# Kernel optimization log

Measured on AMD Instinct MI355X. Metric: run time of the kernel, lower is better.

The kernel has to match this reference:

```python
import jax, jax.numpy as jnp
import numpy as np

N, E, G = 50000, 800000, 256
NODE_IN, EDGE_IN, H, L, RO, OUT = 64, 16, 128, 3, 128, 2
EPS = 1e-5


def _ln(x, g, b):
    m = jnp.mean(x, axis=-1, keepdims=True)
    v = jnp.mean((x - m) ** 2, axis=-1, keepdims=True)
    return (x - m) * jax.lax.rsqrt(v + EPS) * g + b


def setup_inputs() -> dict:
    key = jax.random.key(0)
    ks = iter(jax.random.split(key, 40))
    w = lambda *s: jax.random.normal(next(ks), s, dtype=jnp.float32) * 0.05
    inp = {
        "x": jax.random.normal(next(ks), (N, NODE_IN), dtype=jnp.float32),
        "edge_attr": jax.random.normal(next(ks), (E, EDGE_IN), dtype=jnp.float32),
        "edge_index": jax.random.randint(next(ks), (2, E), 0, N, dtype=jnp.int32),
        "batch": jnp.sort(jax.random.randint(next(ks), (N,), 0, G, dtype=jnp.int32)),
        # encoders + input norms
        "node_enc_w": w(NODE_IN, H), "node_enc_b": jnp.zeros((H,), jnp.float32),
        "edge_enc_w": w(EDGE_IN, H), "edge_enc_b": jnp.zeros((H,), jnp.float32),
        "node_ln_g": jnp.ones((H,), jnp.float32), "node_ln_b": jnp.zeros((H,), jnp.float32),
        "edge_ln_g": jnp.ones((H,), jnp.float32), "edge_ln_b": jnp.zeros((H,), jnp.float32),
        # per-layer stacked params [L, ...]
        "msg_w1": w(L, 2 * H, H), "msg_b1": jnp.zeros((L, H), jnp.float32),
        "msg_w2": w(L, H, H), "msg_b2": jnp.zeros((L, H), jnp.float32),
        "gate_w": w(L, 2 * H, H), "gate_b": jnp.zeros((L, H), jnp.float32),
        "res_w1": w(L, 2 * H, H), "res_b1": jnp.zeros((L, H), jnp.float32),
        "res_w2": w(L, H, H), "res_b2": jnp.zeros((L, H), jnp.float32),
        "ln_g": jnp.ones((L, H), jnp.float32), "ln_b": jnp.zeros((L, H), jnp.float32),
        # readout MLP
        "ro_w1": w(H, RO), "ro_b1": jnp.zeros((RO,), jnp.float32),
        "ro_w2": w(RO, OUT), "ro_b2": jnp.zeros((OUT,), jnp.float32),
    }
    return inp


def reference(x, edge_attr, edge_index, batch,
              node_enc_w, node_enc_b, edge_enc_w, edge_enc_b,
              node_ln_g, node_ln_b, edge_ln_g, edge_ln_b,
              msg_w1, msg_b1, msg_w2, msg_b2, gate_w, gate_b,
              res_w1, res_b1, res_w2, res_b2, ln_g, ln_b,
              ro_w1, ro_b1, ro_w2, ro_b2):
    src, dst = edge_index[0], edge_index[1]
    h = _ln(x @ node_enc_w + node_enc_b, node_ln_g, node_ln_b)        # [N,H]
    e = _ln(edge_attr @ edge_enc_w + edge_enc_b, edge_ln_g, edge_ln_b)  # [E,H]
    for l in range(L):
        cat = jnp.concatenate([h[src], e], axis=-1)                   # [E,2H]
        gate = jax.nn.sigmoid(cat @ gate_w[l] + gate_b[l])
        msg = jax.nn.relu(cat @ msg_w1[l] + msg_b1[l]) @ msg_w2[l] + msg_b2[l]
        agg = jax.ops.segment_sum(gate * msg, dst, num_segments=N)    # scatter-add
        comb = jnp.concatenate([h, agg], axis=-1)                     # [N,2H]
        res = jax.nn.relu(comb @ res_w1[l] + res_b1[l]) @ res_w2[l] + res_b2[l]
        h = _ln(h + res, ln_g[l], ln_b[l])
    # global mean pool over graphs
    sums = jax.ops.segment_sum(h, batch, num_segments=G)              # [G,H]
    cnt = jax.ops.segment_sum(jnp.ones((h.shape[0],), h.dtype), batch, num_segments=G)
    g = sums / jnp.maximum(cnt, 1.0)[:, None]
    return jax.nn.relu(g @ ro_w1 + ro_b1) @ ro_w2 + ro_b2             # [G,OUT]
```

## Files before the change

kernel.cpp:

```cpp
#include <hip/hip_runtime.h>
#include <hip/hip_bf16.h>
#include <math.h>

#define NN 50000
#define NE 800000
#define NG 256
#define H 128
#define NIN 64
#define EIN 16
#define NL 3
#define LEPS 1e-5f

typedef short bf16x8 __attribute__((ext_vector_type(8)));
typedef float f32x4 __attribute__((ext_vector_type(4)));
typedef float f32x16 __attribute__((ext_vector_type(16)));
typedef unsigned u32x4 __attribute__((ext_vector_type(4)));

__device__ __forceinline__ short bf16rne(float x) {
  unsigned u = __float_as_uint(x);
  unsigned r = u + 0x7fff + ((u >> 16) & 1);
  return (short)(r >> 16);
}

__device__ __forceinline__ unsigned pk2(float lo, float hi) {
  __hip_bfloat162 h = __float22bfloat162_rn(make_float2(lo, hi));
  return *(unsigned*)&h;
}

__device__ __forceinline__ float wsum(float v) {
#pragma unroll
  for (int m = 1; m < 64; m <<= 1) v += __shfl_xor(v, m, 64);
  return v;
}

__global__ __launch_bounds__(256) void k_count(const int* __restrict__ eidx,
                                               unsigned* __restrict__ cnt) {
  int t = blockIdx.x * 256 + threadIdx.x;
  if (t < NE) atomicAdd(&cnt[eidx[NE + t]], 1u);
}

__global__ __launch_bounds__(1024) void k_scan(const unsigned* __restrict__ cnt,
                                               unsigned* __restrict__ rowptr) {
  __shared__ unsigned part[16];
  __shared__ unsigned carry_s;
  const int tid = threadIdx.x, lane = tid & 63, wid = tid >> 6;
  if (tid == 0) carry_s = 0;
  __syncthreads();
  for (int base = 0; base < NN; base += 1024) {
    int i = base + tid;
    unsigned v = (i < NN) ? cnt[i] : 0u;
    unsigned incl = v;
#pragma unroll
    for (int off = 1; off < 64; off <<= 1) {
      unsigned t = __shfl_up(incl, off, 64);
      if (lane >= off) incl += t;
    }
    if (lane == 63) part[wid] = incl;
    __syncthreads();
    if (tid == 0) {
      unsigned s = 0;
#pragma unroll
      for (int w = 0; w < 16; w++) { unsigned t = part[w]; part[w] = s; s += t; }
    }
    __syncthreads();
    unsigned carry = carry_s;
    if (i < NN) rowptr[i] = carry + part[wid] + incl - v;
    __syncthreads();
    if (tid == 1023) carry_s = carry + part[15] + incl;
    __syncthreads();
  }
}

__global__ __launch_bounds__(256) void k_fold(
    const float* __restrict__ gate_w, const float* __restrict__ msg_w1,
    const float* __restrict__ gate_b, const float* __restrict__ msg_b1,
    const float* __restrict__ e_enc_w, const float* __restrict__ e_enc_b,
    const float* __restrict__ e_ln_g, const float* __restrict__ e_ln_b,
    short* __restrict__ w2e, float* __restrict__ stats) {
  const int S_W2E = 3 * 8192;
  const int S_ST = S_W2E + 290;
  int tid = blockIdx.x * 256 + threadIdx.x;
  if (tid >= S_ST) return;
  if (tid < S_W2E) {
    int l = tid / 8192, e = tid % 8192;
    int f = e >> 9, lane = (e >> 3) & 63, j = e & 7;
    int nt = f >> 1, ks2 = f & 1;
    int k = ks2 * 16 + (lane >> 5) * 8 + j;
    int n = nt * 32 + (lane & 31);
    float s = 0.f;
    if (k < 19) {
      for (int m = 0; m < 128; m++) {
        float w = (n < 128) ? gate_w[((size_t)l * 256 + 128 + m) * 128 + n]
                            : msg_w1[((size_t)l * 256 + 128 + m) * 128 + (n - 128)];
        float fm = (k < 16)   ? e_enc_w[k * 128 + m] * e_ln_g[m]
                 : (k == 16)  ? e_enc_b[m] * e_ln_g[m]
                 : (k == 17)  ? e_ln_g[m]
                              : e_ln_b[m];
        s += fm * w;
      }
      if (k == 18)
        s += (n < 128) ? gate_b[l * 128 + n] : msg_b1[l * 128 + (n - 128)];
    }
    w2e[tid] = bf16rne(s);
  } else {
    int e = tid - S_W2E;
    if (e < 256) {
      int i = e >> 4, j = e & 15;
      float s = 0.f;
      for (int n = 0; n < 128; n++)
        s += e_enc_w[i * 128 + n] * e_enc_w[j * 128 + n];
      stats[e] = s;
    } else if (e < 272) {
      int k = e - 256;
      float s = 0.f;
      for (int n = 0; n < 128; n++) s += e_enc_w[k * 128 + n];
      stats[e] = s;
    } else if (e < 288) {
      int k = e - 272;
      float s = 0.f;
      for (int n = 0; n < 128; n++) s += e_enc_w[k * 128 + n] * e_enc_b[n];
      stats[e] = s;
    } else if (e == 288) {
      float s = 0.f;
      for (int n = 0; n < 128; n++) s += e_enc_b[n] * e_enc_b[n];
      stats[e] = s;
    } else {
      float s = 0.f;
      for (int n = 0; n < 128; n++) s += e_enc_b[n];
      stats[e] = s;
    }
  }
}

__global__ __launch_bounds__(256) void k_scatter(
    const int* __restrict__ eidx, const float* __restrict__ ea,
    const unsigned* __restrict__ rowptr, unsigned* __restrict__ cursor,
    const float* __restrict__ stats,
    int* __restrict__ src_s, int* __restrict__ dst_s,
    short* __restrict__ ea_bf, float2* __restrict__ rsmu) {
  __shared__ float S[290];
  for (int i = threadIdx.x; i < 290; i += 256) S[i] = stats[i];
  __syncthreads();
  int t = blockIdx.x * 256 + threadIdx.x;
  int s = eidx[t], d = eidx[NE + t];
  unsigned pos = rowptr[d] + atomicAdd(&cursor[d], 1u);
  src_s[pos] = s;
  dst_s[pos] = d;
  const float4* er = (const float4*)(ea + (size_t)t * EIN);
  float4 q0 = er[0], q1 = er[1], q2 = er[2], q3 = er[3];
  float e16[16];
  e16[0]=q0.x; e16[1]=q0.y; e16[2]=q0.z; e16[3]=q0.w;
  e16[4]=q1.x; e16[5]=q1.y; e16[6]=q1.z; e16[7]=q1.w;
  e16[8]=q2.x; e16[9]=q2.y; e16[10]=q2.z; e16[11]=q2.w;
  e16[12]=q3.x; e16[13]=q3.y; e16[14]=q3.z; e16[15]=q3.w;
  short tmp[16];
#pragma unroll
  for (int j = 0; j < 16; j++) tmp[j] = bf16rne(e16[j]);
  short* dstp = ea_bf + (size_t)pos * EIN;
  *(bf16x8*)dstp = *(bf16x8*)tmp;
  *(bf16x8*)(dstp + 8) = *(bf16x8*)(tmp + 8);
  float s1 = S[289], s2 = S[288];
#pragma unroll
  for (int k = 0; k < 16; k++) {
    s1 = fmaf(e16[k], S[256 + k], s1);
    s2 = fmaf(2.f * e16[k], S[272 + k], s2);
  }
#pragma unroll
  for (int i = 0; i < 16; i++) {
    float mi = 0.f;
#pragma unroll
    for (int j = 0; j < 16; j++) mi = fmaf(S[i * 16 + j], e16[j], mi);
    s2 = fmaf(e16[i], mi, s2);
  }
  float mu = s1 * (1.f / 128.f);
  float var = s2 * (1.f / 128.f) - mu * mu;
  float rs = rsqrtf(var + LEPS);
  rsmu[pos] = make_float2(rs, mu);
}

__global__ __launch_bounds__(256) void k_convert_w(
    const float* __restrict__ gate_w, const float* __restrict__ msg_w1,
    const float* __restrict__ msg_w2, const float* __restrict__ res_w1,
    const float* __restrict__ res_w2,
    short* __restrict__ bgh, short* __restrict__ bm2,
    short* __restrict__ brs1, short* __restrict__ brs2) {
  const int S_BGH = 3 * 65536;
  const int S_BM2 = S_BGH + 3 * 16384;
  const int S_BR1 = S_BM2 + 3 * 32768;
  const int S_BR2 = S_BR1 + 3 * 16384;
  int tid = blockIdx.x * 256 + threadIdx.x;
  if (tid >= S_BR2) return;
  if (tid < S_BGH) {
    int l = tid / 65536, e = tid % 65536;
    int f = e >> 9, lane = (e >> 3) & 63, j = e & 7;
    int nt = f >> 4, ks = f & 15;
    int k = ks * 16 + (lane >> 5) * 8 + j;
    int n = nt * 32 + (lane & 31);
    float v = (n < 128) ? gate_w[((size_t)l * 256 + k) * 128 + n]
                        : msg_w1[((size_t)l * 256 + k) * 128 + (n - 128)];
    bgh[tid] = bf16rne(v);
  } else if (tid < S_BM2) {
    int e0 = tid - S_BGH;
    int l = e0 / 16384, e = e0 % 16384;
    int f = e >> 9, lane = (e >> 3) & 63, j = e & 7;
    int nt = f >> 3, ks = f & 7;
    int k = ks * 16 + (lane >> 5) * 8 + j;
    int n = nt * 32 + (lane & 31);
    bm2[e0] = bf16rne(msg_w2[((size_t)l * 128 + k) * 128 + n]);
  } else if (tid < S_BR1) {
    int e0 = tid - S_BM2;
    int l = e0 / 32768, e = e0 % 32768;
    int f = e >> 9, lane = (e >> 3) & 63, j = e & 7;
    int nt = f >> 3, ks = f & 7;
    int k = ks * 32 + (lane >> 4) * 8 + j;
    int n = nt * 16 + (lane & 15);
    brs1[e0] = bf16rne(res_w1[((size_t)l * 256 + k) * 128 + n]);
  } else {
    int e0 = tid - S_BR1;
    int l = e0 / 16384, e = e0 % 16384;
    int f = e >> 9, lane = (e >> 3) & 63, j = e & 7;
    int nt = f >> 2, ks = f & 3;
    int k = ks * 32 + (lane >> 4) * 8 + j;
    int n = nt * 16 + (lane & 15);
    brs2[e0] = bf16rne(res_w2[((size_t)l * 128 + k) * 128 + n]);
  }
}

__global__ __launch_bounds__(256) void k_node_encode(
    const float* __restrict__ x, const float* __restrict__ W,
    const float* __restrict__ bias,
    const float* __restrict__ lng, const float* __restrict__ lnb,
    float* __restrict__ h, short* __restrict__ h_bf) {
  __shared__ float xs[4][8 * NIN];
  const int wave = threadIdx.x >> 6, lane = threadIdx.x & 63;
  const int n0 = (blockIdx.x * 4 + wave) * 8;
  float* xt = xs[wave];
  for (int i = lane; i < 8 * NIN; i += 64) {
    int idx = n0 * NIN + i;
    xt[i] = (idx < NN * NIN) ? x[idx] : 0.f;
  }
  __syncthreads();
  const int c0 = lane, c1 = lane + 64;
  float a0[8], a1[8];
#pragma unroll
  for (int j = 0; j < 8; j++) { a0[j] = 0.f; a1[j] = 0.f; }
  for (int k = 0; k < NIN; k++) {
    float w0 = W[k * H + c0], w1 = W[k * H + c1];
#pragma unroll
    for (int j = 0; j < 8; j++) {
      float xv = xt[j * NIN + k];
      a0[j] = fmaf(xv, w0, a0[j]);
      a1[j] = fmaf(xv, w1, a1[j]);
    }
  }
  const float b0 = bias[c0], b1 = bias[c1];
  const float g0 = lng[c0], g1 = lng[c1], lb0 = lnb[c0], lb1 = lnb[c1];
#pragma unroll
  for (int j = 0; j < 8; j++) {
    float v0 = a0[j] + b0, v1 = a1[j] + b1;
    float mean = wsum(v0 + v1) * (1.f / H);
    float d0 = v0 - mean, d1 = v1 - mean;
    float var = wsum(d0 * d0 + d1 * d1) * (1.f / H);
    float rs = rsqrtf(var + LEPS);
    int n = n0 + j;
    if (n < NN) {
      float o0 = d0 * rs * g0 + lb0, o1 = d1 * rs * g1 + lb1;
      h[n * H + c0] = o0;
      h[n * H + c1] = o1;
      h_bf[n * H + c0] = bf16rne(o0);
      h_bf[n * H + c1] = bf16rne(o1);
    }
  }
}

__global__ __launch_bounds__(256) void k_edge_mfma(
    const short* __restrict__ ea_bf, const float2* __restrict__ rsmu,
    const int* __restrict__ src_s, const int* __restrict__ dst_s,
    const short* __restrict__ h_bf,
    const short* __restrict__ Bgh, const short* __restrict__ Bm2,
    const short* __restrict__ W2e, const float* __restrict__ mbias2,
    float* __restrict__ agg) {
  __shared__ short wbuf[2][4096];
  __shared__ short regn[4][32 * 136];
  __shared__ int dsts[4][32];
  const int tid = threadIdx.x;
  const int wave = tid >> 6, lane = tid & 63;
  const int xcd = blockIdx.x & 7, bidx = blockIdx.x >> 3;
  const int blk = (xcd < 2 ? xcd * 782 : 2 * 782 + (xcd - 2) * 781) + bidx;
  const int e0 = blk * 128 + wave * 32;
  short* R = regn[wave];
  float* Rf = (float*)R;
  const int c31 = lane & 31, halfl = lane >> 5;
  const int koff = halfl * 8;
  const int soff0 = (2 * wave) * 512 + lane * 8;
  const int soff1 = (2 * wave + 1) * 512 + lane * 8;

  if (lane < 32) dsts[wave][lane] = dst_s[e0 + lane];

  bf16x8 w2ef[16];
#pragma unroll
  for (int f = 0; f < 16; f++)
    w2ef[f] = *(const bf16x8*)(W2e + (size_t)(f * 64 + lane) * 8);
  float mb2v[4];
#pragma unroll
  for (int gt = 0; gt < 4; gt++) mb2v[gt] = mbias2[gt * 32 + c31];

  const int srow = src_s[e0 + c31];
  bf16x8 af[8];
#pragma unroll
  for (int ks = 0; ks < 8; ks++)
    af[ks] = *(const bf16x8*)(h_bf + (size_t)srow * H + ks * 16 + koff);

  const float2 rm = rsmu[e0 + c31];
  bf16x8 ae;
  {
    bf16x8 raw = *(const bf16x8*)(ea_bf + (size_t)(e0 + c31) * EIN + koff);
    u32x4 v;
#pragma unroll
    for (int p = 0; p < 4; p++) {
      float lo = __uint_as_float(((unsigned)(unsigned short)raw[2 * p]) << 16) * rm.x;
      float hi = __uint_as_float(((unsigned)(unsigned short)raw[2 * p + 1]) << 16) * rm.x;
      v[p] = pk2(lo, hi);
    }
    ae = __builtin_bit_cast(bf16x8, v);
  }
  bf16x8 ae2;
  {
    u32x4 w;
    w[0] = halfl ? 0u : pk2(rm.x, -rm.x * rm.y);
    w[1] = halfl ? 0u : 0x00003F80u;
    w[2] = 0u; w[3] = 0u;
    ae2 = __builtin_bit_cast(bf16x8, w);
  }

  {
    const short* s = Bgh + (size_t)4 * 8192;
    bf16x8 p0 = *(const bf16x8*)(s + soff0);
    bf16x8 p1 = *(const bf16x8*)(s + soff1);
    *(bf16x8*)&wbuf[0][soff0] = p0;
    *(bf16x8*)&wbuf[0][soff1] = p1;
  }
  __syncthreads();

  bf16x8 a2[8];
  float gate[16];
  bf16x8 sl0, sl1;

#pragma unroll
  for (int t = 0; t < 12; t++) {
    const int b = t & 1;
    if (t < 11) {
      const int tn = t + 1;
      const short* s;
      if (tn < 4) s = Bgh + (size_t)(4 + tn) * 8192;
      else if (((tn - 4) & 1) == 0) s = Bgh + (size_t)((tn - 4) >> 1) * 8192;
      else s = Bm2 + (size_t)((tn - 4) >> 1) * 4096;
      sl0 = *(const bf16x8*)(s + soff0);
      sl1 = *(const bf16x8*)(s + soff1);
    }
    if (t < 4) {
      const int nt = 4 + t;
      __builtin_amdgcn_s_setprio(1);
      f32x16 a = __builtin_amdgcn_mfma_f32_32x32x16_bf16(
          ae, w2ef[nt * 2], (f32x16)(0.f), 0, 0, 0);
      a = __builtin_amdgcn_mfma_f32_32x32x16_bf16(ae2, w2ef[nt * 2 + 1], a, 0, 0, 0);
#pragma unroll
      for (int ks = 0; ks < 8; ks++)
        a = __builtin_amdgcn_mfma_f32_32x32x16_bf16(
            af[ks], *(const bf16x8*)&wbuf[b][ks * 512 + lane * 8], a, 0, 0, 0);
      __builtin_amdgcn_s_setprio(0);
      const int col = t * 32 + c31;
#pragma unroll
      for (int r = 0; r < 16; r++) {
        int row = (r & 3) + 8 * (r >> 2) + 4 * halfl;
        R[row * 136 + col] = bf16rne(fmaxf(a[r], 0.f));
      }
      if (t == 3) {
#pragma unroll
        for (int ks = 0; ks < 8; ks++)
          a2[ks] = *(const bf16x8*)&R[c31 * 136 + ks * 16 + koff];
      }
    } else if (((t - 4) & 1) == 0) {
      const int gt = (t - 4) >> 1;
      __builtin_amdgcn_s_setprio(1);
      f32x16 a = __builtin_amdgcn_mfma_f32_32x32x16_bf16(
          ae, w2ef[gt * 2], (f32x16)(0.f), 0, 0, 0);
      a = __builtin_amdgcn_mfma_f32_32x32x16_bf16(ae2, w2ef[gt * 2 + 1], a, 0, 0, 0);
#pragma unroll
      for (int ks = 0; ks < 8; ks++)
        a = __builtin_amdgcn_mfma_f32_32x32x16_bf16(
            af[ks], *(const bf16x8*)&wbuf[b][ks * 512 + lane * 8], a, 0, 0, 0);
      __builtin_amdgcn_s_setprio(0);
#pragma unroll
      for (int r = 0; r < 16; r++)
        gate[r] = __builtin_amdgcn_rcpf(1.f + __expf(-a[r]));
    } else {
      const int gt = (t - 4) >> 1;
      const int t2 = gt & 1;
      __builtin_amdgcn_s_setprio(1);
      f32x16 m = (f32x16)(0.f);
#pragma unroll
      for (int ks = 0; ks < 8; ks++)
        m = __builtin_amdgcn_mfma_f32_32x32x16_bf16(
            a2[ks], *(const bf16x8*)&wbuf[b][ks * 512 + lane * 8], m, 0, 0, 0);
      __builtin_amdgcn_s_setprio(0);
      const float mb2 = mb2v[gt];
      const int c2 = t2 * 32 + c31;
#pragma unroll
      for (int r = 0; r < 16; r++) {
        int row = (r & 3) + 8 * (r >> 2) + 4 * halfl;
        Rf[row * 68 + c2] = gate[r] * (m[r] + mb2);
      }
      if (t == 7 || t == 11) {
        const int hM = (t == 11);
        const int colg = hM * 64 + lane;
        int cur = dsts[wave][0];
        float run = Rf[lane];
#pragma unroll
        for (int row = 1; row < 32; row++) {
          int d = dsts[wave][row];
          float v = Rf[row * 68 + lane];
          if (d == cur) {
            run += v;
          } else {
            atomicAdd(&agg[(size_t)cur * H + colg], run);
            cur = d; run = v;
          }
        }
        atomicAdd(&agg[(size_t)cur * H + colg], run);
      }
    }
    if (t < 11) {
      *(bf16x8*)&wbuf[b ^ 1][soff0] = sl0;
      *(bf16x8*)&wbuf[b ^ 1][soff1] = sl1;
      __syncthreads();
    }
  }
}

__global__ __launch_bounds__(256) void k_node_up2(
    float* agg, const short* __restrict__ h_bf_in,
    const float* __restrict__ h_in,
    const short* __restrict__ Brs1, const short* __restrict__ Brs2,
    const float* __restrict__ rb1, const float* __restrict__ rb2,
    const float* __restrict__ lng, const float* __restrict__ lnb,
    float* __restrict__ h, short* __restrict__ h_bf) {
  __shared__ short regn[4][16 * 136];
  const int tid = threadIdx.x;
  const int wave = tid >> 6, lane = tid & 63;
  const int xcd = blockIdx.x & 7, bidx = blockIdx.x >> 3;
  const int blk = (xcd < 6 ? xcd * 98 : 6 * 98 + (xcd - 6) * 97) + bidx;
  const int n0 = blk * 64 + wave * 16;
  short* R = regn[wave];
  const int mrow = lane & 15, quad = lane >> 4;

  int nr = n0 + mrow; if (nr >= NN) nr = NN - 1;
  bf16x8 af[8];
#pragma unroll
  for (int ks = 0; ks < 4; ks++)
    af[ks] = *(const bf16x8*)(h_bf_in + (size_t)nr * H + ks * 32 + quad * 8);
#pragma unroll
  for (int ks = 0; ks < 4; ks++) {
    float4 u = *(const float4*)(agg + (size_t)nr * H + ks * 32 + quad * 8);
    float4 w = *(const float4*)(agg + (size_t)nr * H + ks * 32 + quad * 8 + 4);
    short tmp[8];
    tmp[0]=bf16rne(u.x); tmp[1]=bf16rne(u.y); tmp[2]=bf16rne(u.z); tmp[3]=bf16rne(u.w);
    tmp[4]=bf16rne(w.x); tmp[5]=bf16rne(w.y); tmp[6]=bf16rne(w.z); tmp[7]=bf16rne(w.w);
    af[4 + ks] = *(bf16x8*)tmp;
  }
  float4 z4 = make_float4(0.f, 0.f, 0.f, 0.f);
#pragma unroll
  for (int ks = 0; ks < 4; ks++) {
    *(float4*)(agg + (size_t)nr * H + ks * 32 + quad * 8) = z4;
    *(float4*)(agg + (size_t)nr * H + ks * 32 + quad * 8 + 4) = z4;
  }

#pragma unroll
  for (int t = 0; t < 8; t++) {
    f32x4 a = (f32x4){0.f, 0.f, 0.f, 0.f};
#pragma unroll
    for (int ks = 0; ks < 8; ks++) {
      bf16x8 bf = *(const bf16x8*)(Brs1 + (size_t)((t * 8 + ks) * 64 + lane) * 8);
      a = __builtin_amdgcn_mfma_f32_16x16x32_bf16(af[ks], bf, a, 0, 0, 0);
    }
    int col = t * 16 + mrow;
    float b = rb1[col];
#pragma unroll
    for (int r = 0; r < 4; r++)
      R[(quad * 4 + r) * 136 + col] = bf16rne(fmaxf(a[r] + b, 0.f));
  }
  bf16x8 a2[4];
#pragma unroll
  for (int ks = 0; ks < 4; ks++)
    a2[ks] = *(const bf16x8*)&R[mrow * 136 + ks * 32 + quad * 8];

  float vals[8][4];
  float gl[8], bl[8];
#pragma unroll
  for (int t = 0; t < 8; t++) {
    f32x4 a = (f32x4){0.f, 0.f, 0.f, 0.f};
#pragma unroll
    for (int ks = 0; ks < 4; ks++) {
      bf16x8 bf = *(const bf16x8*)(Brs2 + (size_t)((t * 4 + ks) * 64 + lane) * 8);
      a = __builtin_amdgcn_mfma_f32_16x16x32_bf16(a2[ks], bf, a, 0, 0, 0);
    }
    int col = t * 16 + mrow;
    float b2 = rb2[col];
    gl[t] = lng[col]; bl[t] = lnb[col];
#pragma unroll
    for (int r = 0; r < 4; r++) {
      int rowi = n0 + quad * 4 + r;
      int rl = rowi < NN ? rowi : NN - 1;
      vals[t][r] = h_in[(size_t)rl * H + col] + a[r] + b2;
    }
  }
#pragma unroll
  for (int r = 0; r < 4; r++) {
    float s1 = 0.f, s2 = 0.f;
#pragma unroll
    for (int t = 0; t < 8; t++) {
      s1 += vals[t][r];
      s2 = fmaf(vals[t][r], vals[t][r], s2);
    }
#pragma unroll
    for (int m = 1; m < 16; m <<= 1) {
      s1 += __shfl_xor(s1, m, 64);
      s2 += __shfl_xor(s2, m, 64);
    }
    float mean = s1 * (1.f / 128.f);
    float var = s2 * (1.f / 128.f) - mean * mean;
    float rs = rsqrtf(var + LEPS);
    int rowi = n0 + quad * 4 + r;
    if (rowi < NN) {
#pragma unroll
      for (int t = 0; t < 8; t++) {
        int col = t * 16 + mrow;
        float o = (vals[t][r] - mean) * rs * gl[t] + bl[t];
        h[(size_t)rowi * H + col] = o;
        h_bf[(size_t)rowi * H + col] = bf16rne(o);
      }
    }
  }
}

__global__ __launch_bounds__(256) void k_pool(
    const float* __restrict__ h, const int* __restrict__ batch,
    float* __restrict__ gsum, float* __restrict__ gcnt) {
  const int tid = threadIdx.x;
  const int col = tid & 127, half = tid >> 7;
  const int xcd = blockIdx.x & 7, bidx = blockIdx.x >> 3;
  const int blk = (xcd < 3 ? xcd * 196 : 3 * 196 + (xcd - 3) * 195) + bidx;
  int n0 = blk * 32 + half * 16;
  if (n0 >= NN) return;
  int end = n0 + 16; if (end > NN) end = NN;
  int cur = batch[n0];
  float run = h[(size_t)n0 * H + col];
  float cnt = 1.f;
  for (int n = n0 + 1; n < end; n++) {
    int b = batch[n];
    float v = h[(size_t)n * H + col];
    if (b == cur) { run += v; cnt += 1.f; }
    else {
      atomicAdd(&gsum[(size_t)cur * H + col], run);
      if (col == 0) atomicAdd(&gcnt[cur], cnt);
      cur = b; run = v; cnt = 1.f;
    }
  }
  atomicAdd(&gsum[(size_t)cur * H + col], run);
  if (col == 0) atomicAdd(&gcnt[cur], cnt);
}

__global__ __launch_bounds__(128) void k_readout(
    const float* __restrict__ gsum, const float* __restrict__ gcnt,
    const float* __restrict__ W1, const float* __restrict__ b1,
    const float* __restrict__ W2, const float* __restrict__ b2,
    float* __restrict__ out) {
  __shared__ float gs[H];
  __shared__ float o1[H];
  int b = blockIdx.x, c = threadIdx.x;
  float cnt = fmaxf(gcnt[b], 1.f);
  gs[c] = gsum[b * H + c] / cnt;
  __syncthreads();
  float acc = b1[c];
  for (int k = 0; k < H; k++) acc = fmaf(gs[k], W1[k * H + c], acc);
  o1[c] = fmaxf(acc, 0.f);
  __syncthreads();
  if (c < 2) {
    float acc2 = b2[c];
    for (int k = 0; k < H; k++) acc2 = fmaf(o1[k], W2[k * 2 + c], acc2);
    out[b * 2 + c] = acc2;
  }
}

extern "C" void kernel_launch(void* const* d_in, const int* in_sizes, int n_in,
                              void* d_out, int out_size, void* d_ws, size_t ws_size,
                              hipStream_t stream) {
  (void)in_sizes; (void)n_in; (void)out_size; (void)ws_size;
  const float* x       = (const float*)d_in[0];
  const float* ea      = (const float*)d_in[1];
  const int*   eidx    = (const int*)d_in[2];
  const int*   batch   = (const int*)d_in[3];
  const float* n_enc_w = (const float*)d_in[4];
  const float* n_enc_b = (const float*)d_in[5];
  const float* e_enc_w = (const float*)d_in[6];
  const float* e_enc_b = (const float*)d_in[7];
  const float* n_ln_g  = (const float*)d_in[8];
  const float* n_ln_b  = (const float*)d_in[9];
  const float* e_ln_g  = (const float*)d_in[10];
  const float* e_ln_b  = (const float*)d_in[11];
  const float* msg_w1  = (const float*)d_in[12];
  const float* msg_b1  = (const float*)d_in[13];
  const float* msg_w2  = (const float*)d_in[14];
  const float* msg_b2  = (const float*)d_in[15];
  const float* gate_w  = (const float*)d_in[16];
  const float* gate_b  = (const float*)d_in[17];
  const float* res_w1  = (const float*)d_in[18];
  const float* res_b1  = (const float*)d_in[19];
  const float* res_w2  = (const float*)d_in[20];
  const float* res_b2  = (const float*)d_in[21];
  const float* ln_g    = (const float*)d_in[22];
  const float* ln_b    = (const float*)d_in[23];
  const float* ro_w1   = (const float*)d_in[24];
  const float* ro_b1   = (const float*)d_in[25];
  const float* ro_w2   = (const float*)d_in[26];
  const float* ro_b2   = (const float*)d_in[27];

  char* p = (char*)d_ws;
  float* h     = (float*)p;  p += (size_t)NN * H * 4;
  short* h_bf  = (short*)p;  p += (size_t)NN * H * 2;
  float* agg   = (float*)p;  p += (size_t)NN * H * 4;
  short* ea_bf = (short*)p;  p += (size_t)NE * EIN * 2;
  float2* rsmu = (float2*)p; p += (size_t)NE * 8;
  float* gsum  = (float*)p;  p += (size_t)NG * H * 4;
  float* gcnt  = (float*)p;  p += 1024;
  short* bgh   = (short*)p;  p += (size_t)3 * 65536 * 2;
  short* bm2   = (short*)p;  p += (size_t)3 * 16384 * 2;
  short* brs1  = (short*)p;  p += (size_t)3 * 32768 * 2;
  short* brs2  = (short*)p;  p += (size_t)3 * 16384 * 2;
  short* w2e   = (short*)p;  p += (size_t)3 * 8192 * 2;
  float* stats = (float*)p;  p += 2048;
  unsigned* rowptr = (unsigned*)p; p += ((size_t)NN * 4 + 15) / 16 * 16;
  unsigned* cursor = (unsigned*)p; p += ((size_t)NN * 4 + 15) / 16 * 16;
  int* src_s   = (int*)p;    p += (size_t)NE * 4;
  int* dst_s   = (int*)p;    p += (size_t)NE * 4;

  const int node_blocks = (NN + 31) / 32;
  const int nup_blocks  = (NN + 63) / 64;
  const int edge_blocks = NE / 128;
  const int e256 = (NE + 255) / 256;
  const int conv_total = 3 * 65536 + 3 * 16384 + 3 * 32768 + 3 * 16384;
  const int fold_total = 3 * 8192 + 290;

  hipMemsetAsync(cursor, 0, (size_t)NN * 4, stream);
  k_fold<<<(fold_total + 255) / 256, 256, 0, stream>>>(
      gate_w, msg_w1, gate_b, msg_b1, e_enc_w, e_enc_b, e_ln_g, e_ln_b,
      w2e, stats);
  k_count<<<e256, 256, 0, stream>>>(eidx, cursor);
  k_scan<<<1, 1024, 0, stream>>>(cursor, rowptr);
  hipMemsetAsync(cursor, 0, (size_t)NN * 4, stream);
  k_scatter<<<e256, 256, 0, stream>>>(eidx, ea, rowptr, cursor, stats,
                                      src_s, dst_s, ea_bf, rsmu);

  k_convert_w<<<(conv_total + 255) / 256, 256, 0, stream>>>(
      gate_w, msg_w1, msg_w2, res_w1, res_w2,
      bgh, bm2, brs1, brs2);
  k_node_encode<<<node_blocks, 256, 0, stream>>>(x, n_enc_w, n_enc_b, n_ln_g, n_ln_b, h, h_bf);

  hipMemsetAsync(agg, 0, (size_t)NN * H * 4, stream);
  for (int l = 0; l < NL; l++) {
    k_edge_mfma<<<edge_blocks, 256, 0, stream>>>(
        ea_bf, rsmu, src_s, dst_s, h_bf,
        bgh + (size_t)l * 65536, bm2 + (size_t)l * 16384,
        w2e + (size_t)l * 8192, msg_b2 + l * H, agg);
    k_node_up2<<<nup_blocks, 256, 0, stream>>>(
        agg, h_bf, h,
        brs1 + (size_t)l * 32768, brs2 + (size_t)l * 16384,
        res_b1 + l * H, res_b2 + l * H,
        ln_g + l * H, ln_b + l * H, h, h_bf);
  }

  hipMemsetAsync(gsum, 0, ((size_t)NG * H + NG) * 4, stream);
  k_pool<<<(NN + 31) / 32, 256, 0, stream>>>(h, batch, gsum, gcnt);
  k_readout<<<NG, 128, 0, stream>>>(gsum, gcnt, ro_w1, ro_b1, ro_w2, ro_b2, (float*)d_out);
}
```

Before: 901.8 us.

## Swap MFMA operand order so ReLU hidden stays in registers via lane shuffles

```diff
diff --git a/kernel.cpp b/kernel.cpp
--- a/kernel.cpp
+++ b/kernel.cpp
@@ -180,12 +180,12 @@
 
 __global__ __launch_bounds__(256) void k_convert_w(
     const float* __restrict__ gate_w, const float* __restrict__ msg_w1,
-    const float* __restrict__ msg_w2, const float* __restrict__ res_w1,
-    const float* __restrict__ res_w2,
+    const float* __restrict__ msg_w2, const float* __restrict__ msg_b2,
+    const float* __restrict__ res_w1, const float* __restrict__ res_w2,
     short* __restrict__ bgh, short* __restrict__ bm2,
     short* __restrict__ brs1, short* __restrict__ brs2) {
   const int S_BGH = 3 * 65536;
-  const int S_BM2 = S_BGH + 3 * 16384;
+  const int S_BM2 = S_BGH + 3 * 18432;
   const int S_BR1 = S_BM2 + 3 * 32768;
   const int S_BR2 = S_BR1 + 3 * 16384;
   int tid = blockIdx.x * 256 + threadIdx.x;
@@ -201,12 +201,18 @@
     bgh[tid] = bf16rne(v);
   } else if (tid < S_BM2) {
     int e0 = tid - S_BGH;
-    int l = e0 / 16384, e = e0 % 16384;
+    int l = e0 / 18432, e = e0 % 18432;
     int f = e >> 9, lane = (e >> 3) & 63, j = e & 7;
-    int nt = f >> 3, ks = f & 7;
-    int k = ks * 16 + (lane >> 5) * 8 + j;
-    int n = nt * 32 + (lane & 31);
-    bm2[e0] = bf16rne(msg_w2[((size_t)l * 128 + k) * 128 + n]);
+    int gt = f / 9, ks = f % 9;
+    int n = gt * 32 + (lane & 31);
+    float v;
+    if (ks < 8) {
+      int k = ks * 16 + (lane >> 5) * 8 + j;
+      v = msg_w2[((size_t)l * 128 + k) * 128 + n];
+    } else {
+      v = ((lane >> 5) == 0 && j == 0) ? msg_b2[l * 128 + n] : 0.f;
+    }
+    bm2[e0] = bf16rne(v);
   } else if (tid < S_BR1) {
     int e0 = tid - S_BM2;
     int l = e0 / 32768, e = e0 % 32768;
@@ -278,18 +284,16 @@
     const int* __restrict__ src_s, const int* __restrict__ dst_s,
     const short* __restrict__ h_bf,
     const short* __restrict__ Bgh, const short* __restrict__ Bm2,
-    const short* __restrict__ W2e, const float* __restrict__ mbias2,
-    float* __restrict__ agg) {
+    const short* __restrict__ W2e, float* __restrict__ agg) {
   __shared__ short wbuf[2][4096];
-  __shared__ short regn[4][32 * 136];
+  __shared__ float regn[4][32 * 68];
   __shared__ int dsts[4][32];
   const int tid = threadIdx.x;
   const int wave = tid >> 6, lane = tid & 63;
   const int xcd = blockIdx.x & 7, bidx = blockIdx.x >> 3;
   const int blk = (xcd < 2 ? xcd * 782 : 2 * 782 + (xcd - 2) * 781) + bidx;
   const int e0 = blk * 128 + wave * 32;
-  short* R = regn[wave];
-  float* Rf = (float*)R;
+  float* Rf = regn[wave];
   const int c31 = lane & 31, halfl = lane >> 5;
   const int koff = halfl * 8;
   const int soff0 = (2 * wave) * 512 + lane * 8;
@@ -301,9 +305,10 @@
 #pragma unroll
   for (int f = 0; f < 16; f++)
     w2ef[f] = *(const bf16x8*)(W2e + (size_t)(f * 64 + lane) * 8);
-  float mb2v[4];
-#pragma unroll
-  for (int gt = 0; gt < 4; gt++) mb2v[gt] = mbias2[gt * 32 + c31];
+  bf16x8 bm2b[4];
+#pragma unroll
+  for (int gt = 0; gt < 4; gt++)
+    bm2b[gt] = *(const bf16x8*)(Bm2 + (size_t)((gt * 9 + 8) * 64 + lane) * 8);
 
   const int srow = src_s[e0 + c31];
   bf16x8 af[8];
@@ -332,6 +337,13 @@
     w[2] = 0u; w[3] = 0u;
     ae2 = __builtin_bit_cast(bf16x8, w);
   }
+  bf16x8 onefrag;
+  {
+    u32x4 w;
+    w[0] = halfl ? 0u : 0x00003F80u;
+    w[1] = 0u; w[2] = 0u; w[3] = 0u;
+    onefrag = __builtin_bit_cast(bf16x8, w);
+  }
 
   {
     const short* s = Bgh + (size_t)4 * 8192;
@@ -342,7 +354,7 @@
   }
   __syncthreads();
 
-  bf16x8 a2[8];
+  u32x4 a2v[8];
   float gate[16];
   bf16x8 sl0, sl1;
 
@@ -354,7 +366,7 @@
       const short* s;
       if (tn < 4) s = Bgh + (size_t)(4 + tn) * 8192;
       else if (((tn - 4) & 1) == 0) s = Bgh + (size_t)((tn - 4) >> 1) * 8192;
-      else s = Bm2 + (size_t)((tn - 4) >> 1) * 4096;
+      else s = Bm2 + (size_t)((tn - 4) >> 1) * 4608;
       sl0 = *(const bf16x8*)(s + soff0);
       sl1 = *(const bf16x8*)(s + soff1);
     }
@@ -362,34 +374,44 @@
       const int nt = 4 + t;
       __builtin_amdgcn_s_setprio(1);
       f32x16 a = __builtin_amdgcn_mfma_f32_32x32x16_bf16(
-          ae, w2ef[nt * 2], (f32x16)(0.f), 0, 0, 0);
-      a = __builtin_amdgcn_mfma_f32_32x32x16_bf16(ae2, w2ef[nt * 2 + 1], a, 0, 0, 0);
+          w2ef[nt * 2], ae, (f32x16)(0.f), 0, 0, 0);
+      a = __builtin_amdgcn_mfma_f32_32x32x16_bf16(w2ef[nt * 2 + 1], ae2, a, 0, 0, 0);
 #pragma unroll
       for (int ks = 0; ks < 8; ks++)
         a = __builtin_amdgcn_mfma_f32_32x32x16_bf16(
-            af[ks], *(const bf16x8*)&wbuf[b][ks * 512 + lane * 8], a, 0, 0, 0);
+            *(const bf16x8*)&wbuf[b][ks * 512 + lane * 8], af[ks], a, 0, 0, 0);
       __builtin_amdgcn_s_setprio(0);
-      const int col = t * 32 + c31;
-#pragma unroll
-      for (int r = 0; r < 16; r++) {
-        int row = (r & 3) + 8 * (r >> 2) + 4 * halfl;
-        R[row * 136 + col] = bf16rne(fmaxf(a[r], 0.f));
+      unsigned q[8];
+#pragma unroll
+      for (int qq = 0; qq < 4; qq++) {
+        q[2 * qq]     = pk2(fmaxf(a[4 * qq], 0.f),     fmaxf(a[4 * qq + 1], 0.f));
+        q[2 * qq + 1] = pk2(fmaxf(a[4 * qq + 2], 0.f), fmaxf(a[4 * qq + 3], 0.f));
       }
-      if (t == 3) {
-#pragma unroll
-        for (int ks = 0; ks < 8; ks++)
-          a2[ks] = *(const bf16x8*)&R[c31 * 136 + ks * 16 + koff];
-      }
+      unsigned x0a = __shfl_xor(halfl ? q[0] : q[2], 32, 64);
+      unsigned x0b = __shfl_xor(halfl ? q[1] : q[3], 32, 64);
+      unsigned x1a = __shfl_xor(halfl ? q[4] : q[6], 32, 64);
+      unsigned x1b = __shfl_xor(halfl ? q[5] : q[7], 32, 64);
+      u32x4 F0, F1;
+      F0[0] = halfl ? x0a : q[0];
+      F0[1] = halfl ? x0b : q[1];
+      F0[2] = halfl ? q[2] : x0a;
+      F0[3] = halfl ? q[3] : x0b;
+      F1[0] = halfl ? x1a : q[4];
+      F1[1] = halfl ? x1b : q[5];
+      F1[2] = halfl ? q[6] : x1a;
+      F1[3] = halfl ? q[7] : x1b;
+      a2v[2 * t] = F0;
+      a2v[2 * t + 1] = F1;
     } else if (((t - 4) & 1) == 0) {
       const int gt = (t - 4) >> 1;
       __builtin_amdgcn_s_setprio(1);
       f32x16 a = __builtin_amdgcn_mfma_f32_32x32x16_bf16(
-          ae, w2ef[gt * 2], (f32x16)(0.f), 0, 0, 0);
-      a = __builtin_amdgcn_mfma_f32_32x32x16_bf16(ae2, w2ef[gt * 2 + 1], a, 0, 0, 0);
+          w2ef[gt * 2], ae, (f32x16)(0.f), 0, 0, 0);
+      a = __builtin_amdgcn_mfma_f32_32x32x16_bf16(w2ef[gt * 2 + 1], ae2, a, 0, 0, 0);
 #pragma unroll
       for (int ks = 0; ks < 8; ks++)
         a = __builtin_amdgcn_mfma_f32_32x32x16_bf16(
-            af[ks], *(const bf16x8*)&wbuf[b][ks * 512 + lane * 8], a, 0, 0, 0);
+            *(const bf16x8*)&wbuf[b][ks * 512 + lane * 8], af[ks], a, 0, 0, 0);
       __builtin_amdgcn_s_setprio(0);
 #pragma unroll
       for (int r = 0; r < 16; r++)
@@ -402,14 +424,18 @@
 #pragma unroll
       for (int ks = 0; ks < 8; ks++)
         m = __builtin_amdgcn_mfma_f32_32x32x16_bf16(
-            a2[ks], *(const bf16x8*)&wbuf[b][ks * 512 + lane * 8], m, 0, 0, 0);
+            *(const bf16x8*)&wbuf[b][ks * 512 + lane * 8],
+            __builtin_bit_cast(bf16x8, a2v[ks]), m, 0, 0, 0);
+      m = __builtin_amdgcn_mfma_f32_32x32x16_bf16(bm2b[gt], onefrag, m, 0, 0, 0);
       __builtin_amdgcn_s_setprio(0);
-      const float mb2 = mb2v[gt];
-      const int c2 = t2 * 32 + c31;
-#pragma unroll
-      for (int r = 0; r < 16; r++) {
-        int row = (r & 3) + 8 * (r >> 2) + 4 * halfl;
-        Rf[row * 68 + c2] = gate[r] * (m[r] + mb2);
+#pragma unroll
+      for (int qq = 0; qq < 4; qq++) {
+        f32x4 mv;
+        mv[0] = gate[4 * qq] * m[4 * qq];
+        mv[1] = gate[4 * qq + 1] * m[4 * qq + 1];
+        mv[2] = gate[4 * qq + 2] * m[4 * qq + 2];
+        mv[3] = gate[4 * qq + 3] * m[4 * qq + 3];
+        *(f32x4*)&Rf[c31 * 68 + t2 * 32 + qq * 8 + halfl * 4] = mv;
       }
       if (t == 7 || t == 11) {
         const int hM = (t == 11);
@@ -634,7 +660,7 @@
   float* gsum  = (float*)p;  p += (size_t)NG * H * 4;
   float* gcnt  = (float*)p;  p += 1024;
   short* bgh   = (short*)p;  p += (size_t)3 * 65536 * 2;
-  short* bm2   = (short*)p;  p += (size_t)3 * 16384 * 2;
+  short* bm2   = (short*)p;  p += (size_t)3 * 18432 * 2;
   short* brs1  = (short*)p;  p += (size_t)3 * 32768 * 2;
   short* brs2  = (short*)p;  p += (size_t)3 * 16384 * 2;
   short* w2e   = (short*)p;  p += (size_t)3 * 8192 * 2;
@@ -648,7 +674,7 @@
   const int nup_blocks  = (NN + 63) / 64;
   const int edge_blocks = NE / 128;
   const int e256 = (NE + 255) / 256;
-  const int conv_total = 3 * 65536 + 3 * 16384 + 3 * 32768 + 3 * 16384;
+  const int conv_total = 3 * 65536 + 3 * 18432 + 3 * 32768 + 3 * 16384;
   const int fold_total = 3 * 8192 + 290;
 
   hipMemsetAsync(cursor, 0, (size_t)NN * 4, stream);
@@ -662,7 +688,7 @@
                                       src_s, dst_s, ea_bf, rsmu);
 
   k_convert_w<<<(conv_total + 255) / 256, 256, 0, stream>>>(
-      gate_w, msg_w1, msg_w2, res_w1, res_w2,
+      gate_w, msg_w1, msg_w2, msg_b2, res_w1, res_w2,
       bgh, bm2, brs1, brs2);
   k_node_encode<<<node_blocks, 256, 0, stream>>>(x, n_enc_w, n_enc_b, n_ln_g, n_ln_b, h, h_bf);
 
@@ -670,8 +696,8 @@
   for (int l = 0; l < NL; l++) {
     k_edge_mfma<<<edge_blocks, 256, 0, stream>>>(
         ea_bf, rsmu, src_s, dst_s, h_bf,
-        bgh + (size_t)l * 65536, bm2 + (size_t)l * 16384,
-        w2e + (size_t)l * 8192, msg_b2 + l * H, agg);
+        bgh + (size_t)l * 65536, bm2 + (size_t)l * 18432,
+        w2e + (size_t)l * 8192, agg);
     k_node_up2<<<nup_blocks, 256, 0, stream>>>(
         agg, h_bf, h,
         brs1 + (size_t)l * 32768, brs2 + (size_t)l * 16384,
```

Measured after the change: 1.018 ms. 1.13x slower.
